# Optimization experiments

Hardware: AMD Instinct MI355X
Metric: run time of the kernel (lower is better)

Reference implementation:

```python
import jax, jax.numpy as jnp
import numpy as np

NUM_EXPERTS = 64
TOP_K = 2
AUX_COEF = 0.01
Z_COEF = 0.001
INIT_STD = 0.02


def setup_inputs() -> dict:
    key = jax.random.key(0)
    k1, k2 = jax.random.split(key)
    B, S, D = 4, 4096, 2048
    x = jax.random.normal(k1, (B, S, D), dtype=jnp.float32)
    gate_w = jax.random.normal(k2, (NUM_EXPERTS, D), dtype=jnp.float32) * INIT_STD
    return {"x": x, "gate_w": gate_w}


def reference(x, gate_w):
    B, S, D = x.shape
    E, K = NUM_EXPERTS, TOP_K
    # gate linear: (B,S,D) @ (D,E) -> (B,S,E), cast to fp32 like .float()
    logits = jnp.einsum('bsd,ed->bse', x, gate_w).astype(jnp.float32)
    weights = jax.nn.softmax(logits, axis=-1)
    top_weights, top_indices = jax.lax.top_k(weights, K)
    top_weights = top_weights / jnp.sum(top_weights, axis=-1, keepdims=True)
    # load-balance aux loss (training branch)
    flat_idx = top_indices.reshape(-1)
    tokens_per_expert = jax.ops.segment_sum(
        jnp.ones_like(flat_idx, dtype=jnp.float32), flat_idx, num_segments=E)
    f = tokens_per_expert / (B * S * K)
    P = jnp.mean(weights, axis=(0, 1))
    balance_loss = E * jnp.sum(f * P)
    z_loss = jnp.mean(jnp.square(jax.nn.logsumexp(logits, axis=-1)))
    aux_loss = AUX_COEF * balance_loss + Z_COEF * z_loss
    return top_indices, top_weights, aux_loss
```

## Files before the change

### kernel.cpp

```cpp
#include <hip/hip_runtime.h>
#include <math.h>

#define NTOK 16384
#define DDIM 2048
#define NEXP 64
#define MTILE 16
#define KSUP 128
#define NSUP 16

typedef __attribute__((ext_vector_type(8))) short bf16x8;
typedef __attribute__((ext_vector_type(4))) float f32x4;

__device__ __forceinline__ unsigned short f2bf(float f) {
    unsigned int u = __builtin_bit_cast(unsigned int, f);
    u += 0x7fffu + ((u >> 16) & 1u);
    return (unsigned short)(u >> 16);
}
__device__ __forceinline__ float bf2f(unsigned short s) {
    return __builtin_bit_cast(float, ((unsigned int)s) << 16);
}
__device__ __forceinline__ void split3(float x, unsigned short &h,
                                       unsigned short &m, unsigned short &l) {
    h = f2bf(x);
    float r1 = x - bf2f(h);
    m = f2bf(r1);
    float r2 = r1 - bf2f(m);
    l = f2bf(r2);
}

__global__ void k_wpack(const float* __restrict__ gw, unsigned short* __restrict__ wp) {
    int idx = blockIdx.x * 256 + threadIdx.x;
    int lane = idx & 63;
    int ks   = (idx >> 6) & 63;
    int eg   = idx >> 12;
    int e  = eg * 16 + (lane & 15);
    int k0 = ks * 32 + (lane >> 4) * 8;
    const float* src = gw + (size_t)e * DDIM + k0;
    union { unsigned short s[8]; uint4 v; } H, M, L;
    #pragma unroll
    for (int j = 0; j < 8; ++j) split3(src[j], H.s[j], M.s[j], L.s[j]);
    size_t fb = (size_t)(eg * 64 + ks) * 1536 + lane * 8;
    *(uint4*)(wp + fb)        = H.v;
    *(uint4*)(wp + fb + 512)  = M.v;
    *(uint4*)(wp + fb + 1024) = L.v;
}

__device__ __forceinline__ void stage4(char* bb, int srow, int subk, int c, float4 v) {
    unsigned short h0,h1,h2,h3, m0,m1,m2,m3, l0,l1,l2,l3;
    split3(v.x, h0, m0, l0);
    split3(v.y, h1, m1, l1);
    split3(v.z, h2, m2, l2);
    split3(v.w, h3, m3, l3);
    char* pb = bb + srow * 256 + (((c * 8 + (subk >> 1)) ^ srow) << 4)
                  + (subk & 1) * 8;
    *(uint2*)(pb)        = make_uint2((unsigned)h0 | ((unsigned)h1 << 16),
                                      (unsigned)h2 | ((unsigned)h3 << 16));
    *(uint2*)(pb + 4096) = make_uint2((unsigned)m0 | ((unsigned)m1 << 16),
                                      (unsigned)m2 | ((unsigned)m3 << 16));
    *(uint2*)(pb + 8192) = make_uint2((unsigned)l0 | ((unsigned)l1 << 16),
                                      (unsigned)l2 | ((unsigned)l3 << 16));
}

__global__ __launch_bounds__(256, 4)
void k_main(const float* __restrict__ x, const unsigned short* __restrict__ wp,
            float* __restrict__ out, float* __restrict__ gcnt,
            float* __restrict__ gP, float* __restrict__ gz) {
    __shared__ __align__(16) char As[2][12288];
    __shared__ float Lg[MTILE][65];
    __shared__ float Ps[NEXP], Cnt[NEXP], Zs;

    const int tid = threadIdx.x;
    if (tid < NEXP) { Ps[tid] = 0.f; Cnt[tid] = 0.f; }
    if (tid == 0) Zs = 0.f;

    const int tok0 = blockIdx.x * MTILE;
    const int lane = tid & 63;
    const int eg   = __builtin_amdgcn_readfirstlane(tid >> 6);
    const int tau  = lane & 15;
    const int kappa = lane >> 4;

    const int srow = tid >> 4;
    const int subk = tid & 15;
    const float* xb = x + (size_t)(tok0 + srow) * DDIM + subk * 4;

    float4 xc0 = *(const float4*)(xb);
    float4 xc1 = *(const float4*)(xb + 64);
    stage4(As[0], srow, subk, 0, xc0);
    stage4(As[0], srow, subk, 1, xc1);
    xc0 = *(const float4*)(xb + 128);
    xc1 = *(const float4*)(xb + 128 + 64);

    const unsigned short* wpe = wp + (size_t)eg * 64 * 1536 + lane * 8;
    bf16x8 wf[2][3];
    #pragma unroll
    for (int p = 0; p < 3; ++p) wf[0][p] = *(const bf16x8*)(wpe + p * 512);
    #pragma unroll
    for (int p = 0; p < 3; ++p) wf[1][p] = *(const bf16x8*)(wpe + 1536 + p * 512);

    f32x4 acc = {0.f, 0.f, 0.f, 0.f};

    for (int ss = 0; ss < NSUP; ++ss) {
        __syncthreads();
        if (ss + 1 < NSUP) {
            char* nb = As[(ss + 1) & 1];
            stage4(nb, srow, subk, 0, xc0);
            stage4(nb, srow, subk, 1, xc1);
            int nss = (ss + 2) & (NSUP - 1);
            xc0 = *(const float4*)(xb + nss * KSUP);
            xc1 = *(const float4*)(xb + nss * KSUP + 64);
        }
        const char* bb = As[ss & 1];
        #pragma unroll
        for (int ks = 0; ks < 4; ++ks) {
            const char* p0 = bb + tau * 256 + ((((ks << 2) + kappa) ^ tau) << 4);
            bf16x8 Ah = *(const bf16x8*)(p0);
            bf16x8 Am = *(const bf16x8*)(p0 + 4096);
            bf16x8 Al = *(const bf16x8*)(p0 + 8192);
            bf16x8 Bh = wf[ks & 1][0];
            bf16x8 Bm = wf[ks & 1][1];
            bf16x8 Bl = wf[ks & 1][2];

            acc = __builtin_amdgcn_mfma_f32_16x16x32_bf16(Ah, Bh, acc, 0, 0, 0);
            acc = __builtin_amdgcn_mfma_f32_16x16x32_bf16(Ah, Bm, acc, 0, 0, 0);
            acc = __builtin_amdgcn_mfma_f32_16x16x32_bf16(Am, Bh, acc, 0, 0, 0);
            acc = __builtin_amdgcn_mfma_f32_16x16x32_bf16(Ah, Bl, acc, 0, 0, 0);
            acc = __builtin_amdgcn_mfma_f32_16x16x32_bf16(Al, Bh, acc, 0, 0, 0);
            acc = __builtin_amdgcn_mfma_f32_16x16x32_bf16(Am, Bm, acc, 0, 0, 0);

            int nk = ((ss << 2) + ks + 2) & 63;
            #pragma unroll
            for (int pI = 0; pI < 3; ++pI)
                wf[ks & 1][pI] = *(const bf16x8*)(wpe + (size_t)nk * 1536 + pI * 512);
        }
    }

    #pragma unroll
    for (int j = 0; j < 4; ++j)
        Lg[kappa * 4 + j][eg * 16 + tau] = acc[j];
    __syncthreads();

    float Pacc = 0.f, zacc = 0.f;
    const int wv = tid >> 6;
    for (int i = 0; i < 4; ++i) {
        int t = wv * 4 + i;
        float l = Lg[t][lane];
        float mx = l;
        #pragma unroll
        for (int off = 32; off > 0; off >>= 1) mx = fmaxf(mx, __shfl_xor(mx, off));
        float s = expf(l - mx);
        float sum = s;
        #pragma unroll
        for (int off = 32; off > 0; off >>= 1) sum += __shfl_xor(sum, off);
        Pacc += s / sum;

        unsigned long long b1 = __ballot(l == mx);
        int i1 = __ffsll(b1) - 1;
        float l2 = (lane == i1) ? -INFINITY : l;
        float m2 = l2;
        #pragma unroll
        for (int off = 32; off > 0; off >>= 1) m2 = fmaxf(m2, __shfl_xor(m2, off));
        unsigned long long b2 = __ballot(l2 == m2);
        int i2 = __ffsll(b2) - 1;

        if (lane == 0) {
            float s2  = expf(m2 - mx);
            float inv = 1.f / (1.f + s2);
            int gt = tok0 + t;
            ((float2*)out)[gt]              = make_float2((float)i1, (float)i2);
            ((float2*)(out + 2 * NTOK))[gt] = make_float2(inv, s2 * inv);
            atomicAdd(&Cnt[i1], 1.f);
            atomicAdd(&Cnt[i2], 1.f);
            float lse = mx + logf(sum);
            zacc += lse * lse;
        }
    }
    atomicAdd(&Ps[lane], Pacc);
    if (lane == 0) atomicAdd(&Zs, zacc);
    __syncthreads();

    if (tid < NEXP) {
        atomicAdd(&gcnt[tid], Cnt[tid]);
        atomicAdd(&gP[tid],   Ps[tid]);
    }
    if (tid == 0) atomicAdd(gz, Zs);
}

__global__ void k_final(const float* __restrict__ ws, float* __restrict__ out) {
    int lane = threadIdx.x;
    float v = ws[lane] * ws[64 + lane];
    #pragma unroll
    for (int off = 32; off > 0; off >>= 1) v += __shfl_xor(v, off);
    if (lane == 0) {
        float bal = 64.f * v / (32768.f * 16384.f);
        float z   = ws[128] / 16384.f;
        out[4 * NTOK] = 0.01f * bal + 0.001f * z;
    }
}

extern "C" void kernel_launch(void* const* d_in, const int* in_sizes, int n_in,
                              void* d_out, int out_size, void* d_ws, size_t ws_size,
                              hipStream_t stream) {
    const float* x  = (const float*)d_in[0];
    const float* gw = (const float*)d_in[1];
    float* out = (float*)d_out;
    float* wsf = (float*)d_ws;
    unsigned short* wp = (unsigned short*)((char*)d_ws + 1024);

    hipMemsetAsync(d_ws, 0, 516, stream);
    k_wpack<<<64, 256, 0, stream>>>(gw, wp);
    k_main<<<NTOK / MTILE, 256, 0, stream>>>(x, wp, out, wsf, wsf + 64, wsf + 128);
    k_final<<<1, 64, 0, stream>>>(wsf, out);
}
```

Baseline: 86.55 us.

## Split GEMM over K slices with LDS-resident weights and separate reduce kernel

```diff
diff --git a/kernel.cpp b/kernel.cpp
--- a/kernel.cpp
+++ b/kernel.cpp
@@ -4,12 +4,13 @@
 #define NTOK 16384
 #define DDIM 2048
 #define NEXP 64
-#define MTILE 16
-#define KSUP 128
-#define NSUP 16
+#define NKQ 8
+#define KSLICE 256
+#define TPB 128
 
 typedef __attribute__((ext_vector_type(8))) short bf16x8;
 typedef __attribute__((ext_vector_type(4))) float f32x4;
+
 
 __device__ __forceinline__ unsigned short f2bf(float f) {
     unsigned int u = __builtin_bit_cast(unsigned int, f);
@@ -45,105 +46,111 @@
     *(uint4*)(wp + fb + 1024) = L.v;
 }
 
-__device__ __forceinline__ void stage4(char* bb, int srow, int subk, int c, float4 v) {
-    unsigned short h0,h1,h2,h3, m0,m1,m2,m3, l0,l1,l2,l3;
-    split3(v.x, h0, m0, l0);
-    split3(v.y, h1, m1, l1);
-    split3(v.z, h2, m2, l2);
-    split3(v.w, h3, m3, l3);
-    char* pb = bb + srow * 256 + (((c * 8 + (subk >> 1)) ^ srow) << 4)
-                  + (subk & 1) * 8;
-    *(uint2*)(pb)        = make_uint2((unsigned)h0 | ((unsigned)h1 << 16),
-                                      (unsigned)h2 | ((unsigned)h3 << 16));
-    *(uint2*)(pb + 4096) = make_uint2((unsigned)m0 | ((unsigned)m1 << 16),
-                                      (unsigned)m2 | ((unsigned)m3 << 16));
-    *(uint2*)(pb + 8192) = make_uint2((unsigned)l0 | ((unsigned)l1 << 16),
-                                      (unsigned)l2 | ((unsigned)l3 << 16));
-}
-
-__global__ __launch_bounds__(256, 4)
-void k_main(const float* __restrict__ x, const unsigned short* __restrict__ wp,
-            float* __restrict__ out, float* __restrict__ gcnt,
-            float* __restrict__ gP, float* __restrict__ gz) {
-    __shared__ __align__(16) char As[2][12288];
-    __shared__ float Lg[MTILE][65];
+__global__ __launch_bounds__(512, 2)
+void k_gemm(const float* __restrict__ x, const unsigned short* __restrict__ wp,
+            float* __restrict__ part) {
+    __shared__ __align__(16) char Ws[98304];
+
+    const int tid  = threadIdx.x;
+    const int kq   = blockIdx.x & 7;
+    const int tok0 = (blockIdx.x >> 3) * TPB;
+
+    const int lane = tid & 63;
+    const int wv   = tid >> 6;
+    const int tau  = lane & 15;
+    const int kap  = lane >> 4;
+
+    const float* xb = x + (size_t)(tok0 + wv * 16 + tau) * DDIM
+                        + kq * KSLICE + kap * 8;
+    float4 xf[4][2];
+    #pragma unroll
+    for (int i = 0; i < 4; ++i) {
+        xf[i][0] = *(const float4*)(xb + i * 32);
+        xf[i][1] = *(const float4*)(xb + i * 32 + 4);
+    }
+
+    {
+        const char* wpb = (const char*)wp;
+        #pragma unroll
+        for (int eg = 0; eg < 4; ++eg) {
+            const char* s = wpb + (size_t)(eg * 64 + kq * 8) * 3072;
+            char* d = Ws + eg * 24576;
+            #pragma unroll
+            for (int r = 0; r < 3; ++r) {
+                int o = (r * 512 + tid) * 16;
+                *(uint4*)(d + o) = *(const uint4*)(s + o);
+            }
+        }
+    }
+    __syncthreads();
+
+    f32x4 acc[4];
+    #pragma unroll
+    for (int eg = 0; eg < 4; ++eg) acc[eg] = (f32x4){0.f, 0.f, 0.f, 0.f};
+
+    #pragma unroll
+    for (int ks = 0; ks < 8; ++ks) {
+        float4 a = xf[ks & 3][0], b = xf[ks & 3][1];
+        union U8 { unsigned short s[8]; bf16x8 v; };
+        U8 Ah, Am, Al;
+        float in[8] = {a.x, a.y, a.z, a.w, b.x, b.y, b.z, b.w};
+        #pragma unroll
+        for (int j = 0; j < 8; ++j) split3(in[j], Ah.s[j], Am.s[j], Al.s[j]);
+
+        if (ks < 4) {
+            xf[ks & 3][0] = *(const float4*)(xb + (ks + 4) * 32);
+            xf[ks & 3][1] = *(const float4*)(xb + (ks + 4) * 32 + 4);
+        }
+
+        #pragma unroll
+        for (int eg = 0; eg < 4; ++eg) {
+            const char* wb = Ws + eg * 24576 + ks * 3072 + lane * 16;
+            bf16x8 Bh = *(const bf16x8*)(wb);
+            bf16x8 Bm = *(const bf16x8*)(wb + 1024);
+            bf16x8 Bl = *(const bf16x8*)(wb + 2048);
+            acc[eg] = __builtin_amdgcn_mfma_f32_16x16x32_bf16(Ah.v, Bh, acc[eg], 0, 0, 0);
+            acc[eg] = __builtin_amdgcn_mfma_f32_16x16x32_bf16(Ah.v, Bm, acc[eg], 0, 0, 0);
+            acc[eg] = __builtin_amdgcn_mfma_f32_16x16x32_bf16(Am.v, Bh, acc[eg], 0, 0, 0);
+            acc[eg] = __builtin_amdgcn_mfma_f32_16x16x32_bf16(Ah.v, Bl, acc[eg], 0, 0, 0);
+            acc[eg] = __builtin_amdgcn_mfma_f32_16x16x32_bf16(Al.v, Bh, acc[eg], 0, 0, 0);
+            acc[eg] = __builtin_amdgcn_mfma_f32_16x16x32_bf16(Am.v, Bm, acc[eg], 0, 0, 0);
+        }
+    }
+
+    float* pb = part + ((size_t)kq * NTOK + tok0 + wv * 16) * 64;
+    #pragma unroll
+    for (int eg = 0; eg < 4; ++eg)
+        #pragma unroll
+        for (int j = 0; j < 4; ++j)
+            pb[(kap * 4 + j) * 64 + eg * 16 + tau] = acc[eg][j];
+}
+
+__global__ __launch_bounds__(256)
+void k_reduce(const float* __restrict__ part, float* __restrict__ out,
+              float* __restrict__ gcnt, float* __restrict__ gP,
+              float* __restrict__ gz) {
     __shared__ float Ps[NEXP], Cnt[NEXP], Zs;
-
     const int tid = threadIdx.x;
     if (tid < NEXP) { Ps[tid] = 0.f; Cnt[tid] = 0.f; }
     if (tid == 0) Zs = 0.f;
-
-    const int tok0 = blockIdx.x * MTILE;
+    __syncthreads();
+
     const int lane = tid & 63;
-    const int eg   = __builtin_amdgcn_readfirstlane(tid >> 6);
-    const int tau  = lane & 15;
-    const int kappa = lane >> 4;
-
-    const int srow = tid >> 4;
-    const int subk = tid & 15;
-    const float* xb = x + (size_t)(tok0 + srow) * DDIM + subk * 4;
-
-    float4 xc0 = *(const float4*)(xb);
-    float4 xc1 = *(const float4*)(xb + 64);
-    stage4(As[0], srow, subk, 0, xc0);
-    stage4(As[0], srow, subk, 1, xc1);
-    xc0 = *(const float4*)(xb + 128);
-    xc1 = *(const float4*)(xb + 128 + 64);
-
-    const unsigned short* wpe = wp + (size_t)eg * 64 * 1536 + lane * 8;
-    bf16x8 wf[2][3];
-    #pragma unroll
-    for (int p = 0; p < 3; ++p) wf[0][p] = *(const bf16x8*)(wpe + p * 512);
-    #pragma unroll
-    for (int p = 0; p < 3; ++p) wf[1][p] = *(const bf16x8*)(wpe + 1536 + p * 512);
-
-    f32x4 acc = {0.f, 0.f, 0.f, 0.f};
-
-    for (int ss = 0; ss < NSUP; ++ss) {
-        __syncthreads();
-        if (ss + 1 < NSUP) {
-            char* nb = As[(ss + 1) & 1];
-            stage4(nb, srow, subk, 0, xc0);
-            stage4(nb, srow, subk, 1, xc1);
-            int nss = (ss + 2) & (NSUP - 1);
-            xc0 = *(const float4*)(xb + nss * KSUP);
-            xc1 = *(const float4*)(xb + nss * KSUP + 64);
-        }
-        const char* bb = As[ss & 1];
-        #pragma unroll
-        for (int ks = 0; ks < 4; ++ks) {
-            const char* p0 = bb + tau * 256 + ((((ks << 2) + kappa) ^ tau) << 4);
-            bf16x8 Ah = *(const bf16x8*)(p0);
-            bf16x8 Am = *(const bf16x8*)(p0 + 4096);
-            bf16x8 Al = *(const bf16x8*)(p0 + 8192);
-            bf16x8 Bh = wf[ks & 1][0];
-            bf16x8 Bm = wf[ks & 1][1];
-            bf16x8 Bl = wf[ks & 1][2];
-
-            acc = __builtin_amdgcn_mfma_f32_16x16x32_bf16(Ah, Bh, acc, 0, 0, 0);
-            acc = __builtin_amdgcn_mfma_f32_16x16x32_bf16(Ah, Bm, acc, 0, 0, 0);
-            acc = __builtin_amdgcn_mfma_f32_16x16x32_bf16(Am, Bh, acc, 0, 0, 0);
-            acc = __builtin_amdgcn_mfma_f32_16x16x32_bf16(Ah, Bl, acc, 0, 0, 0);
-            acc = __builtin_amdgcn_mfma_f32_16x16x32_bf16(Al, Bh, acc, 0, 0, 0);
-            acc = __builtin_amdgcn_mfma_f32_16x16x32_bf16(Am, Bm, acc, 0, 0, 0);
-
-            int nk = ((ss << 2) + ks + 2) & 63;
-            #pragma unroll
-            for (int pI = 0; pI < 3; ++pI)
-                wf[ks & 1][pI] = *(const bf16x8*)(wpe + (size_t)nk * 1536 + pI * 512);
-        }
-    }
-
-    #pragma unroll
-    for (int j = 0; j < 4; ++j)
-        Lg[kappa * 4 + j][eg * 16 + tau] = acc[j];
-    __syncthreads();
+    const int wv   = tid >> 6;
+    const int t0   = blockIdx.x * 16 + wv * 4;
+
+    float v[4][8];
+    #pragma unroll
+    for (int i = 0; i < 4; ++i)
+        #pragma unroll
+        for (int q = 0; q < 8; ++q)
+            v[i][q] = part[((size_t)q * NTOK + t0 + i) * 64 + lane];
 
     float Pacc = 0.f, zacc = 0.f;
-    const int wv = tid >> 6;
+    #pragma unroll
     for (int i = 0; i < 4; ++i) {
-        int t = wv * 4 + i;
-        float l = Lg[t][lane];
+        float l = ((v[i][0] + v[i][1]) + (v[i][2] + v[i][3]))
+                + ((v[i][4] + v[i][5]) + (v[i][6] + v[i][7]));
         float mx = l;
         #pragma unroll
         for (int off = 32; off > 0; off >>= 1) mx = fmaxf(mx, __shfl_xor(mx, off));
@@ -165,7 +172,7 @@
         if (lane == 0) {
             float s2  = expf(m2 - mx);
             float inv = 1.f / (1.f + s2);
-            int gt = tok0 + t;
+            int gt = t0 + i;
             ((float2*)out)[gt]              = make_float2((float)i1, (float)i2);
             ((float2*)(out + 2 * NTOK))[gt] = make_float2(inv, s2 * inv);
             atomicAdd(&Cnt[i1], 1.f);
@@ -205,9 +212,11 @@
     float* out = (float*)d_out;
     float* wsf = (float*)d_ws;
     unsigned short* wp = (unsigned short*)((char*)d_ws + 1024);
+    float* part = (float*)((char*)d_ws + (1 << 20));
 
     hipMemsetAsync(d_ws, 0, 516, stream);
     k_wpack<<<64, 256, 0, stream>>>(gw, wp);
-    k_main<<<NTOK / MTILE, 256, 0, stream>>>(x, wp, out, wsf, wsf + 64, wsf + 128);
+    k_gemm<<<NKQ * (NTOK / TPB), 512, 0, stream>>>(x, wp, part);
+    k_reduce<<<NTOK / 16, 256, 0, stream>>>(part, out, wsf, wsf + 64, wsf + 128);
     k_final<<<1, 64, 0, stream>>>(wsf, out);
 }
```

Measured after the change: 84.91 us. About the same (-1.9%).
